# Performance work log

Measured on AMD Instinct MI355X. Metric: run time of the kernel, lower is better.

## Reference

```python
import jax, jax.numpy as jnp
import numpy as np

EPS = 1e-6
SCALE_A = 0.9999

def a_powers(A, t):
    # A: [K, n, n]; returns stack [I, A, ..., A^(t-1)] of shape [t, K, n, n] via repeated squaring.
    K, n, _ = A.shape
    eye = jnp.broadcast_to(jnp.eye(n, dtype=A.dtype), (K, n, n))
    result = jnp.stack([eye, A])
    lift = A @ A
    for _ in range(int(np.ceil(np.log2(t))) - 1):
        result = jnp.concatenate([result, result @ lift])
        lift = lift @ lift
    return result[:t]

def fast_conv_real(a, b):
    # a: [len1, K, n, n], b: [batch, len2, K, n] -> conv(b, a): [batch, len1+len2-1, K, n]
    len1 = a.shape[0]
    len2 = b.shape[1]
    T = 2 ** int(np.ceil(np.log2(len1 + len2 - 1)))
    Af = jnp.fft.rfft(a, n=T, axis=0)
    Bf = jnp.fft.rfft(b, n=T, axis=1)
    Cf = jnp.einsum('blki,lkij->blkj', Bf, Af)
    c = jnp.fft.irfft(Cf, n=T, axis=1)
    return c[:, :len1 + len2 - 1]

def rmsnorm(x, w):
    return x * jax.lax.rsqrt(jnp.mean(x * x, axis=-1, keepdims=True) + EPS) * w

def setup_inputs() -> dict:
    key = jax.random.key(0)
    ku, kx, kt, kb, kc = jax.random.split(key, 5)
    batch, length, input_size, state_size, output_size = 8, 4096, 1024, 512, 1024
    K = state_size // 2
    u = jax.random.normal(ku, (batch, length, input_size), dtype=jnp.float32)
    x0 = jax.random.normal(kx, (batch, K, 2), dtype=jnp.float32)
    theta = jax.random.uniform(kt, (K,), dtype=jnp.float32) * (2 * np.pi)
    c, s = jnp.cos(theta), jnp.sin(theta)
    # 2x2 rotation blocks: [[cos, sin], [-sin, cos]], scaled for stability
    A = SCALE_A * jnp.stack([jnp.stack([c, s], -1), jnp.stack([-s, c], -1)], -2)  # [K,2,2]
    B = jax.random.normal(kb, (input_size, state_size), dtype=jnp.float32) / (state_size + input_size) ** 0.5
    C = jax.random.normal(kc, (state_size, output_size), dtype=jnp.float32) / state_size ** 0.5
    norm_weight = jnp.ones((input_size,), dtype=jnp.float32)
    return {"u": u, "x0": x0, "A": A, "B": B, "C": C, "norm_weight": norm_weight}

def reference(u, x0, A, B, C, norm_weight):
    batch, length, _ = u.shape
    K = A.shape[0]
    un = rmsnorm(u, norm_weight)                           # [b, L, in]
    Aps = a_powers(A, length + 1)                          # [L+1, K, 2, 2]
    uB = (un @ B).reshape(batch, length, K, 2)             # [b, L, K, 2]
    x = fast_conv_real(Aps[:-1], uB)[:, :length]           # [b, L, K, 2]
    x = x + jnp.einsum('bki,lkij->blkj', x0, Aps[1:])      # initial-state response
    new_state = x[:, -1]                                   # [b, K, 2]
    y = x.reshape(batch, length, K * 2) @ C                # [b, L, out]
    return y, new_state
```

## Files before the change

### kernel.cpp

```cpp
#include <hip/hip_runtime.h>
#include <hip/hip_bf16.h>

typedef __attribute__((ext_vector_type(8))) short bf16x8;
typedef __attribute__((ext_vector_type(4))) float f32x4;
typedef __attribute__((ext_vector_type(4))) int int4v;

#define BATCH 8
#define LEN 4096
#define DIN 1024
#define DST 512
#define KHALF 256
#define DOUT 1024
#define NCHUNK 64
#define CHUNK 64

static __device__ __forceinline__ ushort f2bf(float f) {
    uint x = __float_as_uint(f);
    uint r = (x + 0x7fffu + ((x >> 16) & 1u)) >> 16;
    return (ushort)r;
}

__global__ __launch_bounds__(256)
void rmsnorm_kernel(const float* __restrict__ u, const float* __restrict__ w,
                    ushort* __restrict__ un)
{
    const int row = blockIdx.x;
    const int t = threadIdx.x;
    const float4 v = ((const float4*)(u + (size_t)row * DIN))[t];
    float ss = v.x*v.x + v.y*v.y + v.z*v.z + v.w*v.w;
    #pragma unroll
    for (int m = 32; m >= 1; m >>= 1) ss += __shfl_xor(ss, m, 64);
    __shared__ float partial[4];
    if ((t & 63) == 0) partial[t >> 6] = ss;
    __syncthreads();
    const float total = partial[0] + partial[1] + partial[2] + partial[3];
    const float scale = rsqrtf(total * (1.0f / DIN) + 1e-6f);
    const float4 wv = ((const float4*)w)[t];
    ushort4 o;
    o.x = f2bf(v.x * scale * wv.x);
    o.y = f2bf(v.y * scale * wv.y);
    o.z = f2bf(v.z * scale * wv.z);
    o.w = f2bf(v.w * scale * wv.w);
    ((ushort4*)(un + (size_t)row * DIN))[t] = o;
}

__global__ __launch_bounds__(256)
void transpose_bf16_kernel(const float* __restrict__ src, ushort* __restrict__ dst,
                           int R, int C)
{
    const int id = blockIdx.x * 256 + threadIdx.x;
    if (id >= R * C) return;
    const int r = id / C, c = id % C;
    dst[(size_t)c * R + r] = f2bf(src[id]);
}

#define BM 128
#define BN 128
#define BK 64
__global__ __launch_bounds__(256, 2)
void gemm_bt_kernel(const ushort* __restrict__ A, const ushort* __restrict__ Bt,
                    float* __restrict__ C, int M, int N, int K)
{
    __shared__ ushort sA[BM * BK];
    __shared__ ushort sB[BN * BK];
    const int tid = threadIdx.x;
    const int lane = tid & 63;
    const int wave = tid >> 6;
    const int wr = wave >> 1, wc = wave & 1;
    const int m0 = blockIdx.x * BM, n0 = blockIdx.y * BN;

    const int sr = tid >> 1;
    const int sh = (tid & 1) * 32;
    const ushort* gA = A + (size_t)(m0 + sr) * K + sh;
    const ushort* gB = Bt + (size_t)(n0 + sr) * K + sh;

    f32x4 acc[4][4] = {};

    const int nkt = K / BK;
    for (int kt = 0; kt < nkt; ++kt) {
        int4v ra[4], rb[4];
        const ushort* pa = gA + kt * BK;
        const ushort* pb = gB + kt * BK;
        #pragma unroll
        for (int j = 0; j < 4; ++j) {
            ra[j] = *(const int4v*)(pa + j * 8);
            rb[j] = *(const int4v*)(pb + j * 8);
        }
        __syncthreads();
        #pragma unroll
        for (int j = 0; j < 4; ++j) {
            const int off = sr * 128 + ((sh * 2 + j * 16) ^ ((sr & 7) << 4));
            *(int4v*)((char*)sA + off) = ra[j];
            *(int4v*)((char*)sB + off) = rb[j];
        }
        __syncthreads();
        #pragma unroll
        for (int kk = 0; kk < 2; ++kk) {
            bf16x8 af[4], bfr[4];
            #pragma unroll
            for (int i = 0; i < 4; ++i) {
                const int arow = wr * 64 + i * 16 + (lane & 15);
                const int aoff = arow * 128 + ((kk * 64 + (lane >> 4) * 16) ^ ((arow & 7) << 4));
                af[i] = *(const bf16x8*)((const char*)sA + aoff);
                const int brow = wc * 64 + i * 16 + (lane & 15);
                const int boff = brow * 128 + ((kk * 64 + (lane >> 4) * 16) ^ ((brow & 7) << 4));
                bfr[i] = *(const bf16x8*)((const char*)sB + boff);
            }
            #pragma unroll
            for (int i = 0; i < 4; ++i)
                #pragma unroll
                for (int j = 0; j < 4; ++j)
                    acc[i][j] = __builtin_amdgcn_mfma_f32_16x16x32_bf16(af[i], bfr[j], acc[i][j], 0, 0, 0);
        }
    }
    #pragma unroll
    for (int i = 0; i < 4; ++i) {
        #pragma unroll
        for (int j = 0; j < 4; ++j) {
            const int row = m0 + wr * 64 + i * 16 + (lane >> 4) * 4;
            const int col = n0 + wc * 64 + j * 16 + (lane & 15);
            float* cp = C + (size_t)row * N + col;
            #pragma unroll
            for (int r = 0; r < 4; ++r)
                cp[(size_t)r * N] = acc[i][j][r];
        }
    }
}

__global__ __launch_bounds__(256)
void scan_local_kernel(const float* __restrict__ uB, const float* __restrict__ A,
                       float* __restrict__ L)
{
    const int c = blockIdx.x, b = blockIdx.y, k = threadIdx.x;
    const float a00 = A[4*k+0], a01 = A[4*k+1], a10 = A[4*k+2], a11 = A[4*k+3];
    const float2* p = (const float2*)uB + ((size_t)b * LEN + c * CHUNK) * KHALF + k;
    float s0 = 0.f, s1 = 0.f;
    #pragma unroll 8
    for (int j = 0; j < CHUNK; ++j) {
        const float2 uv = p[(size_t)j * KHALF];
        const float t0 = fmaf(s0, a00, fmaf(s1, a10, uv.x));
        const float t1 = fmaf(s0, a01, fmaf(s1, a11, uv.y));
        s0 = t0; s1 = t1;
    }
    ((float2*)L)[((size_t)b * NCHUNK + c) * KHALF + k] = make_float2(s0, s1);
}

__global__ __launch_bounds__(256)
void scan_carry_kernel(const float* __restrict__ L, const float* __restrict__ A,
                       const float* __restrict__ x0, float* __restrict__ carry)
{
    const int b = blockIdx.x, k = threadIdx.x;
    float m00 = A[4*k+0], m01 = A[4*k+1], m10 = A[4*k+2], m11 = A[4*k+3];
    #pragma unroll
    for (int i = 0; i < 6; ++i) {
        const float n00 = m00*m00 + m01*m10;
        const float n01 = m00*m01 + m01*m11;
        const float n10 = m10*m00 + m11*m10;
        const float n11 = m10*m01 + m11*m11;
        m00 = n00; m01 = n01; m10 = n10; m11 = n11;
    }
    float c0 = x0[((size_t)b * KHALF + k) * 2 + 0];
    float c1 = x0[((size_t)b * KHALF + k) * 2 + 1];
    for (int c = 0; c < NCHUNK; ++c) {
        ((float2*)carry)[((size_t)b * NCHUNK + c) * KHALF + k] = make_float2(c0, c1);
        const float2 Lc = ((const float2*)L)[((size_t)b * NCHUNK + c) * KHALF + k];
        const float t0 = c0 * m00 + c1 * m10 + Lc.x;
        const float t1 = c0 * m01 + c1 * m11 + Lc.y;
        c0 = t0; c1 = t1;
    }
}

__global__ __launch_bounds__(256)
void scan_final_kernel(const float* __restrict__ uB, const float* __restrict__ A,
                       const float* __restrict__ carry, ushort* __restrict__ xbf,
                       float* __restrict__ state_out)
{
    const int c = blockIdx.x, b = blockIdx.y, k = threadIdx.x;
    const float a00 = A[4*k+0], a01 = A[4*k+1], a10 = A[4*k+2], a11 = A[4*k+3];
    const float2 s = ((const float2*)carry)[((size_t)b * NCHUNK + c) * KHALF + k];
    float s0 = s.x, s1 = s.y;
    const float2* p = (const float2*)uB + ((size_t)b * LEN + c * CHUNK) * KHALF + k;
    uint* xp = (uint*)xbf + ((size_t)b * LEN + c * CHUNK) * KHALF + k;
    #pragma unroll 8
    for (int j = 0; j < CHUNK; ++j) {
        const float2 uv = p[(size_t)j * KHALF];
        const float t0 = fmaf(s0, a00, fmaf(s1, a10, uv.x));
        const float t1 = fmaf(s0, a01, fmaf(s1, a11, uv.y));
        s0 = t0; s1 = t1;
        xp[(size_t)j * KHALF] = (uint)f2bf(s0) | ((uint)f2bf(s1) << 16);
    }
    if (c == NCHUNK - 1) {
        ((float2*)state_out)[(size_t)b * KHALF + k] = make_float2(s0, s1);
    }
}

extern "C" void kernel_launch(void* const* d_in, const int* in_sizes, int n_in,
                              void* d_out, int out_size, void* d_ws, size_t ws_size,
                              hipStream_t stream)
{
    (void)in_sizes; (void)n_in; (void)out_size; (void)ws_size;
    const float* u  = (const float*)d_in[0];
    const float* x0 = (const float*)d_in[1];
    const float* A  = (const float*)d_in[2];
    const float* B  = (const float*)d_in[3];
    const float* C  = (const float*)d_in[4];
    const float* w  = (const float*)d_in[5];
    float* y_out = (float*)d_out;
    float* state_out = y_out + (size_t)BATCH * LEN * DOUT;

    char* ws = (char*)d_ws;
    ushort* un    = (ushort*)(ws + 0);
    ushort* Bt    = (ushort*)(ws + 67108864);
    ushort* Ct    = (ushort*)(ws + 68157440);
    float*  uB    = (float*)(ws + 69206016);
    ushort* xbf   = (ushort*)(ws + 136314880);
    float*  L     = (float*)(ws + 169869312);
    float*  carry = (float*)(ws + 170917888);

    transpose_bf16_kernel<<<dim3((DIN * DST + 255) / 256), 256, 0, stream>>>(B, Bt, DIN, DST);
    transpose_bf16_kernel<<<dim3((DST * DOUT + 255) / 256), 256, 0, stream>>>(C, Ct, DST, DOUT);
    rmsnorm_kernel<<<dim3(BATCH * LEN), 256, 0, stream>>>(u, w, un);
    gemm_bt_kernel<<<dim3(BATCH * LEN / BM, DST / BN), 256, 0, stream>>>(un, Bt, uB, BATCH * LEN, DST, DIN);
    scan_local_kernel<<<dim3(NCHUNK, BATCH), 256, 0, stream>>>(uB, A, L);
    scan_carry_kernel<<<dim3(BATCH), 256, 0, stream>>>(L, A, x0, carry);
    scan_final_kernel<<<dim3(NCHUNK, BATCH), 256, 0, stream>>>(uB, A, carry, xbf, state_out);
    gemm_bt_kernel<<<dim3(BATCH * LEN / BM, DOUT / BN), 256, 0, stream>>>(xbf, Ct, y_out, BATCH * LEN, DOUT, DST);
}
```

Baseline: 377.8 us.

## Load GEMM tiles directly into LDS and swizzle block order for L2 reuse

The GEMM now stages A and B tiles with global_load_lds 16-byte direct-to-LDS loads instead of loading to registers and writing to shared memory. The XOR swizzle moves onto the global source address, so the LDS layout matches what the fragment reads expect. The grid becomes 1D with a remap that groups 8 M-tiles across all N-tiles, so tiles that share operands run close together. Launch bounds rise to 3 blocks per CU to raise occupancy, which tightens the register budget.

```diff
diff --git a/kernel.cpp b/kernel.cpp
--- a/kernel.cpp
+++ b/kernel.cpp
@@ -19,6 +19,10 @@
     uint r = (x + 0x7fffu + ((x >> 16) & 1u)) >> 16;
     return (ushort)r;
 }
+
+#define GL16(gp, lp) __builtin_amdgcn_global_load_lds( \
+    (const __attribute__((address_space(1))) void*)(gp), \
+    (__attribute__((address_space(3))) void*)(lp), 16, 0, 0)
 
 __global__ __launch_bounds__(256)
 void rmsnorm_kernel(const float* __restrict__ u, const float* __restrict__ w,
@@ -57,9 +61,9 @@
 #define BM 128
 #define BN 128
 #define BK 64
-__global__ __launch_bounds__(256, 2)
+__global__ __launch_bounds__(256, 3)
 void gemm_bt_kernel(const ushort* __restrict__ A, const ushort* __restrict__ Bt,
-                    float* __restrict__ C, int M, int N, int K)
+                    float* __restrict__ C, int M, int N, int K, int Nt)
 {
     __shared__ ushort sA[BM * BK];
     __shared__ ushort sB[BN * BK];
@@ -67,31 +71,30 @@
     const int lane = tid & 63;
     const int wave = tid >> 6;
     const int wr = wave >> 1, wc = wave & 1;
-    const int m0 = blockIdx.x * BM, n0 = blockIdx.y * BN;
-
-    const int sr = tid >> 1;
-    const int sh = (tid & 1) * 32;
-    const ushort* gA = A + (size_t)(m0 + sr) * K + sh;
-    const ushort* gB = Bt + (size_t)(n0 + sr) * K + sh;
+
+    const int b = blockIdx.x;
+    const int slot = b >> 3;
+    const int mt = (b & 7) + 8 * (slot / Nt);
+    const int nt = slot - (slot / Nt) * Nt;
+    const int m0 = mt * BM, n0 = nt * BN;
+
+    const size_t K2 = (size_t)K * 2;
+    const int srow = tid >> 3;
+    const int scol = ((tid & 7) << 4) ^ ((srow & 7) << 4);
+    const char* gA = (const char*)A + (size_t)(m0 + srow) * K2 + scol;
+    const char* gB = (const char*)Bt + (size_t)(n0 + srow) * K2 + scol;
+    const int ldsBase = wave * 1024;
 
     f32x4 acc[4][4] = {};
 
     const int nkt = K / BK;
     for (int kt = 0; kt < nkt; ++kt) {
-        int4v ra[4], rb[4];
-        const ushort* pa = gA + kt * BK;
-        const ushort* pb = gB + kt * BK;
+        __syncthreads();
+        const size_t kOff = (size_t)kt * (BK * 2);
         #pragma unroll
-        for (int j = 0; j < 4; ++j) {
-            ra[j] = *(const int4v*)(pa + j * 8);
-            rb[j] = *(const int4v*)(pb + j * 8);
-        }
-        __syncthreads();
-        #pragma unroll
-        for (int j = 0; j < 4; ++j) {
-            const int off = sr * 128 + ((sh * 2 + j * 16) ^ ((sr & 7) << 4));
-            *(int4v*)((char*)sA + off) = ra[j];
-            *(int4v*)((char*)sB + off) = rb[j];
+        for (int c2 = 0; c2 < 4; ++c2) {
+            GL16(gA + (size_t)c2 * 32 * K2 + kOff, (char*)sA + ldsBase + c2 * 4096);
+            GL16(gB + (size_t)c2 * 32 * K2 + kOff, (char*)sB + ldsBase + c2 * 4096);
         }
         __syncthreads();
         #pragma unroll
@@ -220,9 +223,9 @@
     transpose_bf16_kernel<<<dim3((DIN * DST + 255) / 256), 256, 0, stream>>>(B, Bt, DIN, DST);
     transpose_bf16_kernel<<<dim3((DST * DOUT + 255) / 256), 256, 0, stream>>>(C, Ct, DST, DOUT);
     rmsnorm_kernel<<<dim3(BATCH * LEN), 256, 0, stream>>>(u, w, un);
-    gemm_bt_kernel<<<dim3(BATCH * LEN / BM, DST / BN), 256, 0, stream>>>(un, Bt, uB, BATCH * LEN, DST, DIN);
+    gemm_bt_kernel<<<dim3(256 * 4), 256, 0, stream>>>(un, Bt, uB, BATCH * LEN, DST, DIN, 4);
     scan_local_kernel<<<dim3(NCHUNK, BATCH), 256, 0, stream>>>(uB, A, L);
     scan_carry_kernel<<<dim3(BATCH), 256, 0, stream>>>(L, A, x0, carry);
     scan_final_kernel<<<dim3(NCHUNK, BATCH), 256, 0, stream>>>(uB, A, carry, xbf, state_out);
-    gemm_bt_kernel<<<dim3(BATCH * LEN / BM, DOUT / BN), 256, 0, stream>>>(xbf, Ct, y_out, BATCH * LEN, DOUT, DST);
-}
+    gemm_bt_kernel<<<dim3(256 * 8), 256, 0, stream>>>(xbf, Ct, y_out, BATCH * LEN, DOUT, DST, 8);
+}
```

After: 353.1 us. 6.5% less time.
